# Optimization experiments

Hardware: AMD Instinct MI355X
Metric: run time of the kernel (lower is better)

## Reference

```python
import jax, jax.numpy as jnp
import numpy as np

HIDDEN = 1024
HEADS = 16
HEAD = HIDDEN // HEADS


def setup_inputs() -> dict:
    key = jax.random.key(0)
    ks = jax.random.split(key, 10)
    B, T, N = 4, 1024, 1024
    x = jax.random.normal(ks[0], (B, T, HIDDEN), dtype=jnp.float32)
    encoder_feature = jax.random.normal(ks[1], (B, N, HIDDEN), dtype=jnp.float32)
    s = 1.0 / np.sqrt(HIDDEN)
    Wq = jax.random.normal(ks[2], (HIDDEN, HIDDEN), dtype=jnp.float32) * s
    bq = jax.random.normal(ks[3], (HIDDEN,), dtype=jnp.float32) * 0.02
    Wk = jax.random.normal(ks[4], (HIDDEN, HIDDEN), dtype=jnp.float32) * s
    bk = jax.random.normal(ks[5], (HIDDEN,), dtype=jnp.float32) * 0.02
    Wv = jax.random.normal(ks[6], (HIDDEN, HIDDEN), dtype=jnp.float32) * s
    bv = jax.random.normal(ks[7], (HIDDEN,), dtype=jnp.float32) * 0.02
    return {"x": x, "encoder_feature": encoder_feature,
            "Wq": Wq, "bq": bq, "Wk": Wk, "bk": bk, "Wv": Wv, "bv": bv}


def reference(x, encoder_feature, Wq, bq, Wk, bk, Wv, bv):
    B, T, _ = x.shape
    N = encoder_feature.shape[1]
    # torch Linear: y = x @ W.T + b
    q = (x @ Wq.T + bq).reshape(B, T, HEADS, HEAD)
    k = (encoder_feature @ Wk.T + bk).reshape(B, N, HEADS, HEAD)
    v = (encoder_feature @ Wv.T + bv).reshape(B, N, HEADS, HEAD)
    att = jnp.einsum('bthd,bnhd->bhtn', q, k) / jnp.sqrt(jnp.float32(HEAD))
    # causal tril mask sliced to (T, N): position t attends to n <= t
    mask = jnp.tril(jnp.ones((T, N), dtype=bool))
    att = jnp.where(mask[None, None], att, jnp.finfo(att.dtype).min)
    att = jax.nn.softmax(att, axis=-1)
    out = jnp.einsum('bhtn,bnhd->bthd', att, v).reshape(B, T, HIDDEN)
    # NOTE: original forward never applies out_proj; dropout=0.0 (identity)
    return out
```

## Files before the change

### kernel.cpp

```cpp
#include <hip/hip_runtime.h>
#include <hip/hip_bf16.h>
#include <cstdint>
#include <cstddef>

#define B_SZ 4
#define T_SZ 1024
#define N_SZ 1024
#define HID 1024
#define NHEADS 16
#define DHEAD 64

typedef __bf16 bf16x8 __attribute__((ext_vector_type(8)));
typedef __bf16 bf16x4 __attribute__((ext_vector_type(4)));
typedef __bf16 bf16x2 __attribute__((ext_vector_type(2)));
typedef float floatx4 __attribute__((ext_vector_type(4)));
typedef short shortx4 __attribute__((ext_vector_type(4)));

#define LDT 72

#define SM_SCALE_LOG2E 0.18033688011112042f

#define SWZ(row, colbyte) (((row) << 7) + ((((colbyte) + (((row) & 7) << 4))) & 127))

__device__ __forceinline__ void async_copy16(const void* gsrc, void* ldst) {
    __builtin_amdgcn_global_load_lds(
        (const __attribute__((address_space(1))) void*)(uintptr_t)gsrc,
        (__attribute__((address_space(3))) void*)(uintptr_t)ldst, 16, 0, 0);
}

__device__ __forceinline__ floatx4 mfma16bf16(bf16x4 a, bf16x4 b, floatx4 c) {
    shortx4 as = *(shortx4*)&a;
    shortx4 bs = *(shortx4*)&b;
    return __builtin_amdgcn_mfma_f32_16x16x16bf16_1k(as, bs, c, 0, 0, 0);
}

__global__ __launch_bounds__(256)
void cvt6_f32_bf16(const float* __restrict__ x, const float* __restrict__ enc,
                   const float* __restrict__ wq, const float* __restrict__ wk,
                   const float* __restrict__ wv,
                   __bf16* __restrict__ xb, __bf16* __restrict__ eb,
                   __bf16* __restrict__ wqb, __bf16* __restrict__ wkb,
                   __bf16* __restrict__ wvb)
{
    const int job = blockIdx.x;
    const float* s; __bf16* d; int base;
    if (job < 1024)      { s = x;   d = xb;  base = job; }
    else if (job < 2048) { s = enc; d = eb;  base = job - 1024; }
    else if (job < 2304) { s = wq;  d = wqb; base = job - 2048; }
    else if (job < 2560) { s = wk;  d = wkb; base = job - 2304; }
    else                 { s = wv;  d = wvb; base = job - 2560; }

    const size_t off = (size_t)base * 4096 + (size_t)threadIdx.x * 16;
    const float4 a0 = *(const float4*)(s + off);
    const float4 a1 = *(const float4*)(s + off + 4);
    const float4 a2 = *(const float4*)(s + off + 8);
    const float4 a3 = *(const float4*)(s + off + 12);

    bf16x8 o0, o1;
    o0[0] = (__bf16)a0.x; o0[1] = (__bf16)a0.y; o0[2] = (__bf16)a0.z; o0[3] = (__bf16)a0.w;
    o0[4] = (__bf16)a1.x; o0[5] = (__bf16)a1.y; o0[6] = (__bf16)a1.z; o0[7] = (__bf16)a1.w;
    o1[0] = (__bf16)a2.x; o1[1] = (__bf16)a2.y; o1[2] = (__bf16)a2.z; o1[3] = (__bf16)a2.w;
    o1[4] = (__bf16)a3.x; o1[5] = (__bf16)a3.y; o1[6] = (__bf16)a3.z; o1[7] = (__bf16)a3.w;

    *(bf16x8*)(d + off)     = o0;
    *(bf16x8*)(d + off + 8) = o1;
}

#define PBAR() do {                              \
    asm volatile("" ::: "memory");               \
    __builtin_amdgcn_s_barrier();                \
    __builtin_amdgcn_sched_barrier(0);           \
} while (0)

#define MFMA_Q(QM, QN, BREG) do {                                             \
    __builtin_amdgcn_s_setprio(1);                                            \
    _Pragma("unroll")                                                         \
    for (int mf_ = 0; mf_ < 4; ++mf_) {                                       \
        _Pragma("unroll")                                                     \
        for (int nf_ = 0; nf_ < 2; ++nf_) {                                   \
            acc[QM][QN][mf_][nf_] = __builtin_amdgcn_mfma_f32_16x16x32_bf16(  \
                a[mf_][0], BREG[nf_][0], acc[QM][QN][mf_][nf_], 0, 0, 0);     \
            acc[QM][QN][mf_][nf_] = __builtin_amdgcn_mfma_f32_16x16x32_bf16(  \
                a[mf_][1], BREG[nf_][1], acc[QM][QN][mf_][nf_], 0, 0, 0);     \
        }                                                                     \
    }                                                                         \
    __builtin_amdgcn_s_setprio(0);                                            \
} while (0)

#define LOAD_A(BUF, HALF) do {                                                \
    _Pragma("unroll")                                                         \
    for (int mf_ = 0; mf_ < 4; ++mf_) {                                       \
        a[mf_][0] = ldsA(BUF, HALF, mf_, 0);                                  \
        a[mf_][1] = ldsA(BUF, HALF, mf_, 1);                                  \
    }                                                                         \
} while (0)

#define LOAD_B(DST, BUF, HALF) do {                                           \
    _Pragma("unroll")                                                         \
    for (int nf_ = 0; nf_ < 2; ++nf_) {                                       \
        DST[nf_][0] = ldsB(BUF, HALF, nf_, 0);                                \
        DST[nf_][1] = ldsB(BUF, HALF, nf_, 1);                                \
    }                                                                         \
} while (0)

__global__ __launch_bounds__(512, 2)
void gemm3_256_8ph(const __bf16* __restrict__ xb, const __bf16* __restrict__ eb,
                   const __bf16* __restrict__ wqb, const __bf16* __restrict__ wkb,
                   const __bf16* __restrict__ wvb,
                   const float* __restrict__ bq, const float* __restrict__ bk,
                   const float* __restrict__ bv,
                   __bf16* __restrict__ qo, __bf16* __restrict__ ko,
                   __bf16* __restrict__ vo)
{
    __shared__ __align__(16) __bf16 AS[2][2][8192];
    __shared__ __align__(16) __bf16 BS[2][2][8192];

    const int bid = blockIdx.x;
    const int swz = (bid & 7) * 24 + (bid >> 3);
    const int mt  = swz >> 2;
    const int nt  = swz & 3;
    const int z   = mt >> 4;
    const int bm  = (mt & 15) << 8;
    const int bn  = nt << 8;

    const __bf16* A; const __bf16* W; const float* bias; __bf16* C;
    if (z == 0)      { A = xb; W = wqb; bias = bq; C = qo; }
    else if (z == 1) { A = eb; W = wkb; bias = bk; C = ko; }
    else             { A = eb; W = wvb; bias = bv; C = vo; }

    const int tid  = threadIdx.x;
    const int lane = tid & 63;
    const int wid  = tid >> 6;
    const int l15  = lane & 15;
    const int quad = lane >> 4;
    const int wmid = wid >> 2;
    const int wnid = wid & 3;

    const int sr  = tid >> 3;
    const int sch = tid & 7;

    auto stage2 = [&](const __bf16* src, __bf16* dst, int gRow0, int kt) {
        const int c = (sch ^ (sr & 7)) << 3;
        async_copy16(src + (size_t)(gRow0 + sr) * HID + kt * 64 + c,
                     (char*)dst + tid * 16);
        async_copy16(src + (size_t)(gRow0 + sr + 64) * HID + kt * 64 + c,
                     (char*)dst + 8192 + tid * 16);
    };

    auto ldsA = [&](int buf, int half, int mf, int kk) -> bf16x8 {
        const int r = wmid * 64 + mf * 16 + l15;
        return *(const bf16x8*)((const char*)&AS[buf][half][0] + r * 128 +
                                (((kk * 4 + quad) ^ (r & 7)) << 4));
    };
    auto ldsB = [&](int buf, int half, int nf, int kk) -> bf16x8 {
        const int r = wnid * 32 + nf * 16 + l15;
        return *(const bf16x8*)((const char*)&BS[buf][half][0] + r * 128 +
                                (((kk * 4 + quad) ^ (r & 7)) << 4));
    };

    bf16x8 a[4][2], b0[2][2], b1[2][2];
    floatx4 acc[2][2][4][2];
#pragma unroll
    for (int i = 0; i < 2; ++i)
#pragma unroll
        for (int j = 0; j < 2; ++j)
#pragma unroll
            for (int m = 0; m < 4; ++m)
#pragma unroll
                for (int n = 0; n < 2; ++n)
                    acc[i][j][m][n] = (floatx4)(0.0f);

    stage2(A, &AS[0][0][0], bm,       0);
    stage2(W, &BS[0][0][0], bn,       0);
    stage2(W, &BS[0][1][0], bn + 128, 0);
    stage2(A, &AS[0][1][0], bm + 128, 0);
    stage2(A, &AS[1][0][0], bm,       1);
    stage2(W, &BS[1][0][0], bn,       1);
    stage2(W, &BS[1][1][0], bn + 128, 1);
    asm volatile("s_waitcnt vmcnt(6)" ::: "memory");
    PBAR();

#pragma unroll 1
    for (int it = 0; it < 8; ++it) {
        const int kt1 = 2 * it + 1;
        const int kta = (it < 7) ? 2 * it + 2 : 14;
        const int ktb = (it < 7) ? 2 * it + 3 : 15;

        LOAD_A(0, 0);
        LOAD_B(b0, 0, 0);
        stage2(A, &AS[1][1][0], bm + 128, kt1);
        PBAR();
        MFMA_Q(0, 0, b0);
        PBAR();
        LOAD_B(b1, 0, 1);
        stage2(A, &AS[0][0][0], bm, kta);
        PBAR();
        MFMA_Q(0, 1, b1);
        PBAR();
        LOAD_A(0, 1);
        stage2(W, &BS[0][0][0], bn, kta);
        PBAR();
        MFMA_Q(1, 1, b1);
        PBAR();
        stage2(W, &BS[0][1][0], bn + 128, kta);
        PBAR();
        MFMA_Q(1, 0, b0);
        asm volatile("s_waitcnt vmcnt(6)" ::: "memory");
        PBAR();
        LOAD_A(1, 0);
        LOAD_B(b0, 1, 0);
        stage2(A, &AS[0][1][0], bm + 128, kta);
        PBAR();
        MFMA_Q(0, 0, b0);
        PBAR();
        LOAD_B(b1, 1, 1);
        stage2(A, &AS[1][0][0], bm, ktb);
        PBAR();
        MFMA_Q(0, 1, b1);
        PBAR();
        LOAD_A(1, 1);
        stage2(W, &BS[1][0][0], bn, ktb);
        PBAR();
        MFMA_Q(1, 1, b1);
        PBAR();
        stage2(W, &BS[1][1][0], bn + 128, ktb);
        PBAR();
        MFMA_Q(1, 0, b0);
        asm volatile("s_waitcnt vmcnt(6)" ::: "memory");
        PBAR();
    }

#pragma unroll
    for (int qn = 0; qn < 2; ++qn)
#pragma unroll
        for (int nf = 0; nf < 2; ++nf) {
            const int n = bn + qn * 128 + wnid * 32 + nf * 16 + l15;
            const float bias_f = bias[n];
#pragma unroll
            for (int qm = 0; qm < 2; ++qm)
#pragma unroll
                for (int mf = 0; mf < 4; ++mf) {
                    const int m0 = bm + qm * 128 + wmid * 64 + mf * 16 + quad * 4;
#pragma unroll
                    for (int r = 0; r < 4; ++r)
                        C[(size_t)(m0 + r) * HID + n] =
                            (__bf16)(acc[qm][qn][mf][nf][r] + bias_f);
                }
        }
}

#undef LOAD_A
#undef LOAD_B
#undef MFMA_Q
#undef PBAR

__global__ __launch_bounds__(256)
void gemm_bt_bias_f32in(const float* __restrict__ A,
                        const float* __restrict__ W,
                        const float* __restrict__ bias,
                        __hip_bfloat16* __restrict__ C)
{
    constexpr int K = HID;
    __shared__ __align__(16) __hip_bfloat16 As[128 * LDT];
    __shared__ __align__(16) __hip_bfloat16 Bs[128 * LDT];

    const int tid  = threadIdx.x;
    const int wave = tid >> 6;
    const int lane = tid & 63;
    const int bm = blockIdx.y * 128;
    const int bn = blockIdx.x * 128;
    const int wm = (wave >> 1) * 64;
    const int wn = (wave & 1) * 64;

    floatx4 acc[4][4];
#pragma unroll
    for (int i = 0; i < 4; ++i)
#pragma unroll
        for (int j = 0; j < 4; ++j)
            acc[i][j] = (floatx4)(0.0f);

    const int lr = tid >> 4;
    const int lc = (tid & 15) * 4;

    for (int k0 = 0; k0 < K; k0 += 64) {
#pragma unroll
        for (int qq = 0; qq < 8; ++qq) {
            const int r = lr + qq * 16;
            const float4 a4 = *(const float4*)(A + (size_t)(bm + r) * K + k0 + lc);
            const float4 w4 = *(const float4*)(W + (size_t)(bn + r) * K + k0 + lc);
            bf16x4 av, wv;
            av[0] = (__bf16)a4.x; av[1] = (__bf16)a4.y; av[2] = (__bf16)a4.z; av[3] = (__bf16)a4.w;
            wv[0] = (__bf16)w4.x; wv[1] = (__bf16)w4.y; wv[2] = (__bf16)w4.z; wv[3] = (__bf16)w4.w;
            *(bf16x4*)(As + r * LDT + lc) = av;
            *(bf16x4*)(Bs + r * LDT + lc) = wv;
        }
        __syncthreads();
#pragma unroll
        for (int kk = 0; kk < 2; ++kk) {
            const int krow = kk * 32 + (lane >> 4) * 8;
            const int mrow = wm + (lane & 15);
            const int nrow = wn + (lane & 15);
            bf16x8 af[4], bfr[4];
#pragma unroll
            for (int i = 0; i < 4; ++i) {
                af[i]  = *(const bf16x8*)(As + (mrow + i * 16) * LDT + krow);
                bfr[i] = *(const bf16x8*)(Bs + (nrow + i * 16) * LDT + krow);
            }
#pragma unroll
            for (int mi = 0; mi < 4; ++mi)
#pragma unroll
                for (int ni = 0; ni < 4; ++ni)
                    acc[mi][ni] = __builtin_amdgcn_mfma_f32_16x16x32_bf16(
                        af[mi], bfr[ni], acc[mi][ni], 0, 0, 0);
        }
        __syncthreads();
    }

    const int crow0 = bm + wm + (lane >> 4) * 4;
    const int ccol0 = bn + wn + (lane & 15);
#pragma unroll
    for (int ni = 0; ni < 4; ++ni) {
        const int n = ccol0 + ni * 16;
        const float bias_f = bias[n];
#pragma unroll
        for (int mi = 0; mi < 4; ++mi) {
#pragma unroll
            for (int r = 0; r < 4; ++r) {
                const int m = crow0 + mi * 16 + r;
                C[(size_t)m * HID + n] = __float2bfloat16(acc[mi][ni][r] + bias_f);
            }
        }
    }
}

__global__ __launch_bounds__(256, 4)
void attn_flash_mfma_v6(const __bf16* __restrict__ q,
                        const __bf16* __restrict__ k,
                        const __bf16* __restrict__ v,
                        float* __restrict__ out)
{
    __shared__ __align__(16) char Ks[2][64 * 128];
    __shared__ __align__(16) char Vt[2][64 * 128];

    const int tid  = threadIdx.x;
    const int wave = tid >> 6;
    const int lane = tid & 63;
    const int l15  = lane & 15;
    const int quad = lane >> 4;

    const int bx = blockIdx.x;
    const int jj = bx & 15;
    const int bt = ((bx >> 8) & 1) ? jj : 15 - jj;
    const int bh = bx >> 4;
    const int h  = bh & (NHEADS - 1);
    const int b  = bh >> 4;
    const int t0 = bt * 64;

    const __bf16* kbase = k + (size_t)b * N_SZ * HID + h * DHEAD;
    const __bf16* vbase = v + (size_t)b * N_SZ * HID + h * DHEAD;

    bf16x8 qf[2];
    {
        const __bf16* qb = q + (size_t)(b * T_SZ + t0 + wave * 16 + l15) * HID + h * DHEAD;
#pragma unroll
        for (int kk = 0; kk < 2; ++kk) {
            const bf16x8 raw = *(const bf16x8*)(qb + kk * 32 + quad * 8);
#pragma unroll
            for (int j = 0; j < 8; ++j)
                qf[kk][j] = (__bf16)((float)raw[j] * SM_SCALE_LOG2E);
        }
    }

    const int kr  = tid >> 3;
    const int kce = (tid & 7) * 8;
    const int vn2 = (tid & 31) * 2;
    const int vd2 = (tid >> 5) * 8;

    {
        *(bf16x8*)(&Ks[0][0] + SWZ(kr, kce * 2)) =
            *(const bf16x8*)(kbase + (size_t)kr * HID + kce);
        *(bf16x8*)(&Ks[0][0] + SWZ(kr + 32, kce * 2)) =
            *(const bf16x8*)(kbase + (size_t)(kr + 32) * HID + kce);
        const bf16x8 va = *(const bf16x8*)(vbase + (size_t)vn2 * HID + vd2);
        const bf16x8 vb = *(const bf16x8*)(vbase + (size_t)(vn2 + 1) * HID + vd2);
#pragma unroll
        for (int j = 0; j < 8; ++j) {
            bf16x2 t2; t2[0] = va[j]; t2[1] = vb[j];
            *(bf16x2*)(&Vt[0][0] + SWZ(vd2 + j, vn2 * 2)) = t2;
        }
    }
    __syncthreads();

    float lsum = 0.f;
    floatx4 oacc[4];
#pragma unroll
    for (int nd = 0; nd < 4; ++nd) oacc[nd] = (floatx4)(0.0f);

    const int ntiles = bt + 1;
    const int tq = t0 + wave * 16 + l15;

    for (int it = 0; it < ntiles; ++it) {
        const int bi = it & 1;
        const int n0 = it * 64;

        bf16x8 nk0, nk1, nva, nvb;
        const bool pf = (it + 1 < ntiles);
        if (pf) {
            const int nn0 = n0 + 64;
            nk0 = *(const bf16x8*)(kbase + (size_t)(nn0 + kr) * HID + kce);
            nk1 = *(const bf16x8*)(kbase + (size_t)(nn0 + kr + 32) * HID + kce);
            nva = *(const bf16x8*)(vbase + (size_t)(nn0 + vn2) * HID + vd2);
            nvb = *(const bf16x8*)(vbase + (size_t)(nn0 + vn2 + 1) * HID + vd2);
        }

        floatx4 st[4];
#pragma unroll
        for (int ni = 0; ni < 4; ++ni) st[ni] = (floatx4)(0.0f);
        const char* ksb = &Ks[bi][0];
        __builtin_amdgcn_s_setprio(1);
#pragma unroll
        for (int kk = 0; kk < 2; ++kk) {
            const int cb = kk * 64 + quad * 16;
#pragma unroll
            for (int ni = 0; ni < 4; ++ni) {
                const bf16x8 af = *(const bf16x8*)(ksb + SWZ(ni * 16 + l15, cb));
                st[ni] = __builtin_amdgcn_mfma_f32_16x16x32_bf16(af, qf[kk], st[ni], 0, 0, 0);
            }
        }
        __builtin_amdgcn_s_setprio(0);

        const bool msk = (it == bt);
        bf16x4 pa[4];
#pragma unroll
        for (int ni = 0; ni < 4; ++ni) {
            bf16x4 pk;
#pragma unroll
            for (int r = 0; r < 4; ++r) {
                float p = exp2f(st[ni][r]);
                if (msk) {
                    const int nn = n0 + ni * 16 + quad * 4 + r;
                    p = (nn > tq) ? 0.f : p;
                }
                lsum += p;
                pk[r] = (__bf16)p;
            }
            pa[ni] = pk;
        }

        const char* vtb = &Vt[bi][0];
        __builtin_amdgcn_s_setprio(1);
#pragma unroll
        for (int ni = 0; ni < 4; ++ni) {
            const int cb = ni * 32 + quad * 8;
#pragma unroll
            for (int nd = 0; nd < 4; ++nd) {
                const bf16x4 av = *(const bf16x4*)(vtb + SWZ(nd * 16 + l15, cb));
                oacc[nd] = mfma16bf16(av, pa[ni], oacc[nd]);
            }
        }
        __builtin_amdgcn_s_setprio(0);

        if (pf) {
            char* kd = &Ks[bi ^ 1][0];
            char* vd = &Vt[bi ^ 1][0];
            *(bf16x8*)(kd + SWZ(kr, kce * 2)) = nk0;
            *(bf16x8*)(kd + SWZ(kr + 32, kce * 2)) = nk1;
#pragma unroll
            for (int j = 0; j < 8; ++j) {
                bf16x2 t2; t2[0] = nva[j]; t2[1] = nvb[j];
                *(bf16x2*)(vd + SWZ(vd2 + j, vn2 * 2)) = t2;
            }
        }
        __syncthreads();
    }

    lsum += __shfl_xor(lsum, 16, 64);
    lsum += __shfl_xor(lsum, 32, 64);
    {
        const float invl = 1.0f / lsum;
        float* ob = out + (size_t)(b * T_SZ + tq) * HID + h * DHEAD + quad * 4;
#pragma unroll
        for (int nd = 0; nd < 4; ++nd) {
            float4 o4;
            o4.x = oacc[nd][0] * invl;
            o4.y = oacc[nd][1] * invl;
            o4.z = oacc[nd][2] * invl;
            o4.w = oacc[nd][3] * invl;
            *(float4*)(ob + nd * 16) = o4;
        }
    }
}

extern "C" void kernel_launch(void* const* d_in, const int* in_sizes, int n_in,
                              void* d_out, int out_size, void* d_ws, size_t ws_size,
                              hipStream_t stream) {
    const float* x   = (const float*)d_in[0];
    const float* enc = (const float*)d_in[1];
    const float* Wq  = (const float*)d_in[2];
    const float* bq  = (const float*)d_in[3];
    const float* Wk  = (const float*)d_in[4];
    const float* bk  = (const float*)d_in[5];
    const float* Wv  = (const float*)d_in[6];
    const float* bv  = (const float*)d_in[7];
    float* out = (float*)d_out;

    char* ws = (char*)d_ws;
    const size_t MiB = 1024 * 1024;
    __bf16* q_ws = (__bf16*)(ws);
    __bf16* k_ws = (__bf16*)(ws + 8 * MiB);
    __bf16* v_ws = (__bf16*)(ws + 16 * MiB);

    const dim3 blk(256);
    if (ws_size >= 46 * MiB) {
        __bf16* xb  = (__bf16*)(ws + 24 * MiB);
        __bf16* eb  = (__bf16*)(ws + 32 * MiB);
        __bf16* wqb = (__bf16*)(ws + 40 * MiB);
        __bf16* wkb = (__bf16*)(ws + 42 * MiB);
        __bf16* wvb = (__bf16*)(ws + 44 * MiB);
        cvt6_f32_bf16<<<dim3(2816), blk, 0, stream>>>(x, enc, Wq, Wk, Wv,
                                                      xb, eb, wqb, wkb, wvb);
        gemm3_256_8ph<<<dim3(192), dim3(512), 0, stream>>>(
            xb, eb, wqb, wkb, wvb, bq, bk, bv, q_ws, k_ws, v_ws);
    } else {
        const dim3 gg(HID / 128, (B_SZ * T_SZ) / 128);
        gemm_bt_bias_f32in<<<gg, blk, 0, stream>>>(x,   Wq, bq, (__hip_bfloat16*)q_ws);
        gemm_bt_bias_f32in<<<gg, blk, 0, stream>>>(enc, Wk, bk, (__hip_bfloat16*)k_ws);
        gemm_bt_bias_f32in<<<gg, blk, 0, stream>>>(enc, Wv, bv, (__hip_bfloat16*)v_ws);
    }

    attn_flash_mfma_v6<<<dim3(1024), blk, 0, stream>>>(q_ws, k_ws, v_ws, out);
}
```

Before: 154.5 us.

## Replace LDS-staged pipelined QKV GEMM with direct global-to-register MFMA loads

The QKV projection GEMM drops its double-buffered LDS staging, async global-to-LDS copies and barrier-phased schedule. Each wave now loads its A and W fragments straight from global memory into registers every k-step and relies on L2/cache reuse across waves. This removes barriers and LDS traffic, but every wave fetches its operands from global memory separately with strided 16-byte loads and no explicit prefetch. That likely exposes memory latency and raises cache traffic.

```diff
diff --git a/kernel.cpp b/kernel.cpp
--- a/kernel.cpp
+++ b/kernel.cpp
@@ -21,12 +21,6 @@
 #define SM_SCALE_LOG2E 0.18033688011112042f
 
 #define SWZ(row, colbyte) (((row) << 7) + ((((colbyte) + (((row) & 7) << 4))) & 127))
-
-__device__ __forceinline__ void async_copy16(const void* gsrc, void* ldst) {
-    __builtin_amdgcn_global_load_lds(
-        (const __attribute__((address_space(1))) void*)(uintptr_t)gsrc,
-        (__attribute__((address_space(3))) void*)(uintptr_t)ldst, 16, 0, 0);
-}
 
 __device__ __forceinline__ floatx4 mfma16bf16(bf16x4 a, bf16x4 b, floatx4 c) {
     shortx4 as = *(shortx4*)&a;
@@ -66,55 +60,15 @@
     *(bf16x8*)(d + off + 8) = o1;
 }
 
-#define PBAR() do {                              \
-    asm volatile("" ::: "memory");               \
-    __builtin_amdgcn_s_barrier();                \
-    __builtin_amdgcn_sched_barrier(0);           \
-} while (0)
-
-#define MFMA_Q(QM, QN, BREG) do {                                             \
-    __builtin_amdgcn_s_setprio(1);                                            \
-    _Pragma("unroll")                                                         \
-    for (int mf_ = 0; mf_ < 4; ++mf_) {                                       \
-        _Pragma("unroll")                                                     \
-        for (int nf_ = 0; nf_ < 2; ++nf_) {                                   \
-            acc[QM][QN][mf_][nf_] = __builtin_amdgcn_mfma_f32_16x16x32_bf16(  \
-                a[mf_][0], BREG[nf_][0], acc[QM][QN][mf_][nf_], 0, 0, 0);     \
-            acc[QM][QN][mf_][nf_] = __builtin_amdgcn_mfma_f32_16x16x32_bf16(  \
-                a[mf_][1], BREG[nf_][1], acc[QM][QN][mf_][nf_], 0, 0, 0);     \
-        }                                                                     \
-    }                                                                         \
-    __builtin_amdgcn_s_setprio(0);                                            \
-} while (0)
-
-#define LOAD_A(BUF, HALF) do {                                                \
-    _Pragma("unroll")                                                         \
-    for (int mf_ = 0; mf_ < 4; ++mf_) {                                       \
-        a[mf_][0] = ldsA(BUF, HALF, mf_, 0);                                  \
-        a[mf_][1] = ldsA(BUF, HALF, mf_, 1);                                  \
-    }                                                                         \
-} while (0)
-
-#define LOAD_B(DST, BUF, HALF) do {                                           \
-    _Pragma("unroll")                                                         \
-    for (int nf_ = 0; nf_ < 2; ++nf_) {                                       \
-        DST[nf_][0] = ldsB(BUF, HALF, nf_, 0);                                \
-        DST[nf_][1] = ldsB(BUF, HALF, nf_, 1);                                \
-    }                                                                         \
-} while (0)
-
 __global__ __launch_bounds__(512, 2)
-void gemm3_256_8ph(const __bf16* __restrict__ xb, const __bf16* __restrict__ eb,
-                   const __bf16* __restrict__ wqb, const __bf16* __restrict__ wkb,
-                   const __bf16* __restrict__ wvb,
-                   const float* __restrict__ bq, const float* __restrict__ bk,
-                   const float* __restrict__ bv,
-                   __bf16* __restrict__ qo, __bf16* __restrict__ ko,
-                   __bf16* __restrict__ vo)
+void gemm3_l2(const __bf16* __restrict__ xb, const __bf16* __restrict__ eb,
+              const __bf16* __restrict__ wqb, const __bf16* __restrict__ wkb,
+              const __bf16* __restrict__ wvb,
+              const float* __restrict__ bq, const float* __restrict__ bk,
+              const float* __restrict__ bv,
+              __bf16* __restrict__ qo, __bf16* __restrict__ ko,
+              __bf16* __restrict__ vo)
 {
-    __shared__ __align__(16) __bf16 AS[2][2][8192];
-    __shared__ __align__(16) __bf16 BS[2][2][8192];
-
     const int bid = blockIdx.x;
     const int swz = (bid & 7) * 24 + (bid >> 3);
     const int mt  = swz >> 2;
@@ -136,123 +90,54 @@
     const int wmid = wid >> 2;
     const int wnid = wid & 3;
 
-    const int sr  = tid >> 3;
-    const int sch = tid & 7;
-
-    auto stage2 = [&](const __bf16* src, __bf16* dst, int gRow0, int kt) {
-        const int c = (sch ^ (sr & 7)) << 3;
-        async_copy16(src + (size_t)(gRow0 + sr) * HID + kt * 64 + c,
-                     (char*)dst + tid * 16);
-        async_copy16(src + (size_t)(gRow0 + sr + 64) * HID + kt * 64 + c,
-                     (char*)dst + 8192 + tid * 16);
-    };
-
-    auto ldsA = [&](int buf, int half, int mf, int kk) -> bf16x8 {
-        const int r = wmid * 64 + mf * 16 + l15;
-        return *(const bf16x8*)((const char*)&AS[buf][half][0] + r * 128 +
-                                (((kk * 4 + quad) ^ (r & 7)) << 4));
-    };
-    auto ldsB = [&](int buf, int half, int nf, int kk) -> bf16x8 {
-        const int r = wnid * 32 + nf * 16 + l15;
-        return *(const bf16x8*)((const char*)&BS[buf][half][0] + r * 128 +
-                                (((kk * 4 + quad) ^ (r & 7)) << 4));
-    };
-
-    bf16x8 a[4][2], b0[2][2], b1[2][2];
-    floatx4 acc[2][2][4][2];
-#pragma unroll
-    for (int i = 0; i < 2; ++i)
-#pragma unroll
-        for (int j = 0; j < 2; ++j)
-#pragma unroll
-            for (int m = 0; m < 4; ++m)
-#pragma unroll
-                for (int n = 0; n < 2; ++n)
-                    acc[i][j][m][n] = (floatx4)(0.0f);
-
-    stage2(A, &AS[0][0][0], bm,       0);
-    stage2(W, &BS[0][0][0], bn,       0);
-    stage2(W, &BS[0][1][0], bn + 128, 0);
-    stage2(A, &AS[0][1][0], bm + 128, 0);
-    stage2(A, &AS[1][0][0], bm,       1);
-    stage2(W, &BS[1][0][0], bn,       1);
-    stage2(W, &BS[1][1][0], bn + 128, 1);
-    asm volatile("s_waitcnt vmcnt(6)" ::: "memory");
-    PBAR();
-
-#pragma unroll 1
-    for (int it = 0; it < 8; ++it) {
-        const int kt1 = 2 * it + 1;
-        const int kta = (it < 7) ? 2 * it + 2 : 14;
-        const int ktb = (it < 7) ? 2 * it + 3 : 15;
-
-        LOAD_A(0, 0);
-        LOAD_B(b0, 0, 0);
-        stage2(A, &AS[1][1][0], bm + 128, kt1);
-        PBAR();
-        MFMA_Q(0, 0, b0);
-        PBAR();
-        LOAD_B(b1, 0, 1);
-        stage2(A, &AS[0][0][0], bm, kta);
-        PBAR();
-        MFMA_Q(0, 1, b1);
-        PBAR();
-        LOAD_A(0, 1);
-        stage2(W, &BS[0][0][0], bn, kta);
-        PBAR();
-        MFMA_Q(1, 1, b1);
-        PBAR();
-        stage2(W, &BS[0][1][0], bn + 128, kta);
-        PBAR();
-        MFMA_Q(1, 0, b0);
-        asm volatile("s_waitcnt vmcnt(6)" ::: "memory");
-        PBAR();
-        LOAD_A(1, 0);
-        LOAD_B(b0, 1, 0);
-        stage2(A, &AS[0][1][0], bm + 128, kta);
-        PBAR();
-        MFMA_Q(0, 0, b0);
-        PBAR();
-        LOAD_B(b1, 1, 1);
-        stage2(A, &AS[1][0][0], bm, ktb);
-        PBAR();
-        MFMA_Q(0, 1, b1);
-        PBAR();
-        LOAD_A(1, 1);
-        stage2(W, &BS[1][0][0], bn, ktb);
-        PBAR();
-        MFMA_Q(1, 1, b1);
-        PBAR();
-        stage2(W, &BS[1][1][0], bn + 128, ktb);
-        PBAR();
-        MFMA_Q(1, 0, b0);
-        asm volatile("s_waitcnt vmcnt(6)" ::: "memory");
-        PBAR();
-    }
-
-#pragma unroll
-    for (int qn = 0; qn < 2; ++qn)
-#pragma unroll
-        for (int nf = 0; nf < 2; ++nf) {
-            const int n = bn + qn * 128 + wnid * 32 + nf * 16 + l15;
-            const float bias_f = bias[n];
-#pragma unroll
-            for (int qm = 0; qm < 2; ++qm)
-#pragma unroll
-                for (int mf = 0; mf < 4; ++mf) {
-                    const int m0 = bm + qm * 128 + wmid * 64 + mf * 16 + quad * 4;
-#pragma unroll
-                    for (int r = 0; r < 4; ++r)
-                        C[(size_t)(m0 + r) * HID + n] =
-                            (__bf16)(acc[qm][qn][mf][nf][r] + bias_f);
-                }
-        }
-}
-
-#undef LOAD_A
-#undef LOAD_B
-#undef MFMA_Q
-#undef PBAR
+    const __bf16* pa[8];
+    const __bf16* pb[4];
+#pragma unroll
+    for (int rg = 0; rg < 8; ++rg) {
+        const int row = bm + (rg >> 2) * 128 + wmid * 64 + (rg & 3) * 16 + l15;
+        pa[rg] = A + (size_t)row * HID + quad * 8;
+    }
+#pragma unroll
+    for (int cg = 0; cg < 4; ++cg) {
+        const int row = bn + (cg >> 1) * 128 + wnid * 32 + (cg & 1) * 16 + l15;
+        pb[cg] = W + (size_t)row * HID + quad * 8;
+    }
+
+    floatx4 acc[8][4];
+#pragma unroll
+    for (int rg = 0; rg < 8; ++rg)
+#pragma unroll
+        for (int cg = 0; cg < 4; ++cg)
+            acc[rg][cg] = (floatx4)(0.0f);
+
+#pragma unroll 2
+    for (int k0 = 0; k0 < HID; k0 += 32) {
+        bf16x8 af[8], bf[4];
+#pragma unroll
+        for (int rg = 0; rg < 8; ++rg) af[rg] = *(const bf16x8*)(pa[rg] + k0);
+#pragma unroll
+        for (int cg = 0; cg < 4; ++cg) bf[cg] = *(const bf16x8*)(pb[cg] + k0);
+#pragma unroll
+        for (int rg = 0; rg < 8; ++rg)
+#pragma unroll
+            for (int cg = 0; cg < 4; ++cg)
+                acc[rg][cg] = __builtin_amdgcn_mfma_f32_16x16x32_bf16(
+                    af[rg], bf[cg], acc[rg][cg], 0, 0, 0);
+    }
+
+#pragma unroll
+    for (int cg = 0; cg < 4; ++cg) {
+        const int n = bn + (cg >> 1) * 128 + wnid * 32 + (cg & 1) * 16 + l15;
+        const float bias_f = bias[n];
+#pragma unroll
+        for (int rg = 0; rg < 8; ++rg) {
+            const int m0 = bm + (rg >> 2) * 128 + wmid * 64 + (rg & 3) * 16 + quad * 4;
+#pragma unroll
+            for (int r = 0; r < 4; ++r)
+                C[(size_t)(m0 + r) * HID + n] = (__bf16)(acc[rg][cg][r] + bias_f);
+        }
+    }
+}
 
 __global__ __launch_bounds__(256)
 void gemm_bt_bias_f32in(const float* __restrict__ A,
@@ -519,7 +404,7 @@
         __bf16* wvb = (__bf16*)(ws + 44 * MiB);
         cvt6_f32_bf16<<<dim3(2816), blk, 0, stream>>>(x, enc, Wq, Wk, Wv,
                                                       xb, eb, wqb, wkb, wvb);
-        gemm3_256_8ph<<<dim3(192), dim3(512), 0, stream>>>(
+        gemm3_l2<<<dim3(192), dim3(512), 0, stream>>>(
             xb, eb, wqb, wkb, wvb, bq, bk, bv, q_ws, k_ws, v_ws);
     } else {
         const dim3 gg(HID / 128, (B_SZ * T_SZ) / 128);
```

Result: slower. 215.4 us (+39.4%).
